# Kernel optimization log

Hardware: AMD Instinct MI355X
Metric: run time of the kernel (lower is better)

The kernel has to match this reference:

```python
import jax, jax.numpy as jnp
import numpy as np

B, T, C, H = 4, 2048, 1024, 16
D = C // H  # head_dim = 64


def setup_inputs() -> dict:
    key = jax.random.key(0)
    ks = jax.random.split(key, 5)
    s = 0.02
    return {
        "x": jax.random.normal(ks[0], (B, T, C), dtype=jnp.float32),
        "w_qkv": jax.random.normal(ks[1], (C, 3 * C), dtype=jnp.float32) * s,
        "b_qkv": jnp.zeros((3 * C,), dtype=jnp.float32),
        "w_proj": jax.random.normal(ks[2], (C, C), dtype=jnp.float32) * s,
        "b_proj": jnp.zeros((C,), dtype=jnp.float32),
    }


def reference(x, w_qkv, b_qkv, w_proj, b_proj):
    Bx, Tx, Cx = x.shape
    qkv = x @ w_qkv + b_qkv                      # [B,T,3C]
    q, k, v = jnp.split(qkv, 3, axis=-1)
    # [B,T,C] -> [B,H,T,D]
    q = q.reshape(Bx, Tx, H, D).transpose(0, 2, 1, 3)
    k = k.reshape(Bx, Tx, H, D).transpose(0, 2, 1, 3)
    v = v.reshape(Bx, Tx, H, D).transpose(0, 2, 1, 3)
    scale = 1.0 / np.sqrt(D).astype(np.float32)
    attn = jnp.einsum('bhqd,bhkd->bhqk', q, k) * scale   # [B,H,T,T]
    causal = jnp.tril(jnp.ones((Tx, Tx), dtype=bool))
    attn = jnp.where(causal[None, None], attn, -jnp.inf)
    attn = jax.nn.softmax(attn, axis=-1)
    out = jnp.einsum('bhqk,bhkd->bhqd', attn, v)          # [B,H,T,D]
    out = out.transpose(0, 2, 1, 3).reshape(Bx, Tx, Cx)   # [B,T,C]
    return out @ w_proj + b_proj
```

## Files before the change

kernel.cpp:

```cpp
#include <hip/hip_runtime.h>
#include <hip/hip_bf16.h>
#include <math.h>

using bf16 = __hip_bfloat16;
typedef __bf16 bf16x8 __attribute__((ext_vector_type(8)));
typedef float  f32x4  __attribute__((ext_vector_type(4)));
typedef unsigned short ushort8 __attribute__((ext_vector_type(8)));
typedef unsigned uint2v __attribute__((ext_vector_type(2)));

#define DEV __device__ __forceinline__

DEV void gld_lds16(const void* g, void* l) {
    __builtin_amdgcn_global_load_lds((const __attribute__((address_space(1))) void*)g,
                                     (__attribute__((address_space(3))) void*)l,
                                     16, 0, 0);
}

__global__ __launch_bounds__(256) void cast_f32_bf16(const float* __restrict__ in,
                                                     bf16* __restrict__ out, int n4) {
    int i = blockIdx.x * blockDim.x + threadIdx.x;
    if (i >= n4) return;
    float4 f = ((const float4*)in)[i];
    __align__(8) bf16 o[4] = {__float2bfloat16(f.x), __float2bfloat16(f.y),
                              __float2bfloat16(f.z), __float2bfloat16(f.w)};
    ((uint64_t*)out)[i] = *(const uint64_t*)o;
}

__global__ __launch_bounds__(256) void transpose_cast(const float* __restrict__ in,
                                                      bf16* __restrict__ out, int R, int Cn) {
    __shared__ float tile[32][33];
    int bx = blockIdx.x * 32;
    int by = blockIdx.y * 32;
    int tx = threadIdx.x & 31, ty = threadIdx.x >> 5;
    for (int i = ty; i < 32; i += 8)
        tile[i][tx] = in[(size_t)(by + i) * Cn + bx + tx];
    __syncthreads();
    for (int i = ty; i < 32; i += 8)
        out[(size_t)(bx + i) * R + by + tx] = __float2bfloat16(tile[tx][i]);
}

__global__ __launch_bounds__(256) void gemm_qkv(const bf16* __restrict__ A,
                                                const bf16* __restrict__ Bt,
                                                const float* __restrict__ bias,
                                                bf16* __restrict__ qb,
                                                bf16* __restrict__ kb,
                                                bf16* __restrict__ vTb) {
    constexpr int K = 1024, T = 2048;
    constexpr float CS = 0.18033688f;
    __shared__ __align__(16) bf16 Al[128 * 32];
    __shared__ __align__(16) bf16 Bl[128 * 32];
    __shared__ __align__(16) bf16 Et[32 * 136];
    int tid = threadIdx.x;
    int lane = tid & 63, w = tid >> 6;
    int wm = w >> 1, wn = w & 1;
    int l15 = lane & 15, quad = lane >> 4;
    int m0 = blockIdx.x * 128, n0 = blockIdx.y * 128;
    int l3 = l15 & 3;

    f32x4 acc[4][4] = {};
    for (int k0 = 0; k0 < K; k0 += 32) {
        __syncthreads();
        for (int it = 0; it < 2; ++it) {
            int e = (it * 256 + tid) * 8;
            int r = e >> 5, cu = (e >> 3) & 3;
            int cs = ((cu ^ (r & 3)) << 3);
            gld_lds16(A  + (size_t)(m0 + r) * K + k0 + cs, &Al[e]);
            gld_lds16(Bt + (size_t)(n0 + r) * K + k0 + cs, &Bl[e]);
        }
        __syncthreads();
        bf16x8 af[4], bfr[4];
        for (int i = 0; i < 4; ++i)
            af[i] = *(const bf16x8*)&Al[(wm * 64 + i * 16 + l15) * 32 + ((quad ^ l3) << 3)];
        for (int j = 0; j < 4; ++j)
            bfr[j] = *(const bf16x8*)&Bl[(wn * 64 + j * 16 + l15) * 32 + ((quad ^ l3) << 3)];
        for (int i = 0; i < 4; ++i)
            for (int j = 0; j < 4; ++j)
                acc[i][j] = __builtin_amdgcn_mfma_f32_16x16x32_bf16(af[i], bfr[j], acc[i][j], 0, 0, 0);
    }

    int mode = (blockIdx.y < 8) ? 0 : (blockIdx.y < 16 ? 1 : 2);
    float bv[4];
    for (int j = 0; j < 4; ++j)
        bv[j] = bias[n0 + wn * 64 + j * 16 + l15];
    float scl = (mode == 0) ? CS : 1.0f;

    for (int i = 0; i < 4; ++i) {
        __syncthreads();
        for (int j = 0; j < 4; ++j)
            for (int v = 0; v < 4; ++v)
                Et[(wm * 16 + quad * 4 + v) * 136 + wn * 64 + j * 16 + l15] =
                    __float2bfloat16((acc[i][j][v] + bv[j]) * scl);
        __syncthreads();
        if (mode < 2) {
            int r = tid >> 3, cc = (tid & 7) * 16;
            int m = m0 + i * 16 + (r < 16 ? r : r + 48);
            int b = m >> 11, t = m & 2047;
            int n = (n0 & 1023) + cc;
            int h = n >> 6, d = n & 63;
            bf16* dst = (mode == 0 ? qb : kb) + (((size_t)(b * 16 + h)) * T + t) * 64 + d;
            ushort8 u0 = *(const ushort8*)&Et[r * 136 + cc];
            ushort8 u1 = *(const ushort8*)&Et[r * 136 + cc + 8];
            *(ushort8*)dst = u0;
            *(ushort8*)(dst + 8) = u1;
        } else {
            int run = tid >> 7, d = tid & 127;
            int t0 = m0 + i * 16 + run * 64;
            int b = t0 >> 11, tt = t0 & 2047;
            int n = (n0 & 1023) + d;
            int h = n >> 6, dd = n & 63;
            __align__(16) bf16 tmp[16];
            for (int jj = 0; jj < 16; ++jj)
                tmp[jj] = Et[(run * 16 + jj) * 136 + d];
            bf16* dst = vTb + (((size_t)(b * 16 + h)) * 64 + dd) * T + tt;
            *(ushort8*)dst = *(const ushort8*)tmp;
            *(ushort8*)(dst + 8) = *(const ushort8*)(tmp + 8);
        }
    }
}

__global__ __launch_bounds__(256, 4) void flash_attn(const bf16* __restrict__ qb,
                                                     const bf16* __restrict__ kbuf,
                                                     const bf16* __restrict__ vT,
                                                     bf16* __restrict__ ob) {
    constexpr int T = 2048;
    __shared__ __align__(16) bf16 Kl[2][64 * 64];
    __shared__ __align__(16) bf16 Vl[64 * 64];
    __shared__ __align__(16) bf16 Pl[128 * 64];
    int tid = threadIdx.x;
    int lane = tid & 63, w = tid >> 6;
    int l15 = lane & 15, quad = lane >> 4;

    int g = blockIdx.x;
    int quarter = g >> 8;
    int j = (g >> 6) & 3;
    int bh = g & 63;
    int xq;
    switch (quarter) {
        case 0:  xq = 15 - j; break;
        case 1:  xq = 8 + j;  break;
        case 2:  xq = 4 + j;  break;
        default: xq = 3 - j;  break;
    }
    int q0 = xq << 7;
    const bf16* qbase = qb   + (size_t)bh * T * 64;
    const bf16* kbase = kbuf + (size_t)bh * T * 64;
    const bf16* vbase = vT   + (size_t)bh * 64 * T;

    int qg[2];
    bf16x8 qa[2][2];
#pragma unroll
    for (int s = 0; s < 2; ++s) {
        qg[s] = q0 + w * 32 + s * 16 + l15;
#pragma unroll
        for (int c = 0; c < 2; ++c)
            qa[s][c] = *(const bf16x8*)(qbase + (size_t)qg[s] * 64 + c * 32 + quad * 8);
    }

    bf16x8 ones;
#pragma unroll
    for (int i = 0; i < 8; ++i) ones[i] = (__bf16)1.0f;

    f32x4 O[2][4] = {};
    f32x4 O1[2] = {};
    int h7 = l15 & 7;

    int off0 = tid * 8, off1 = (256 + tid) * 8;
    int r0 = off0 >> 6, cb0 = (off0 >> 3) & 7;
    int r1 = off1 >> 6, cb1 = (off1 >> 3) & 7;
    int kc0 = (cb0 ^ (r0 & 7)) << 3, kc1 = (cb1 ^ (r1 & 7)) << 3;

    int prow0 = w * 32 + l15;
    int nit = 2 * xq + 2;

    bf16x8 vr0 = *(const bf16x8*)(vbase + (size_t)r0 * T + kc0);
    bf16x8 vr1 = *(const bf16x8*)(vbase + (size_t)r1 * T + kc1);
    gld_lds16(kbase + (size_t)r0 * 64 + kc0, &Kl[0][off0]);
    gld_lds16(kbase + (size_t)r1 * 64 + kc1, &Kl[0][off1]);
    *(bf16x8*)&Vl[off0] = vr0;
    *(bf16x8*)&Vl[off1] = vr1;

    for (int t = 0; t < nit; ++t) {
        int cur = t & 1;
        __syncthreads();
        bool pre = (t + 1 < nit);
        if (pre) {
            int kb2 = (t + 1) << 6, nxt = cur ^ 1;
            vr0 = *(const bf16x8*)(vbase + (size_t)r0 * T + kb2 + kc0);
            vr1 = *(const bf16x8*)(vbase + (size_t)r1 * T + kb2 + kc1);
            gld_lds16(kbase + (size_t)(kb2 + r0) * 64 + kc0, &Kl[nxt][off0]);
            gld_lds16(kbase + (size_t)(kb2 + r1) * 64 + kc1, &Kl[nxt][off1]);
        }
        int kb = t << 6;
        bool maskt = (t >= nit - 2);

#pragma unroll
        for (int jn = 0; jn < 4; ++jn) {
            int row = jn * 16 + l15;
            bf16x8 a0 = *(const bf16x8*)&Kl[cur][row * 64 + ((quad ^ h7) << 3)];
            bf16x8 a1 = *(const bf16x8*)&Kl[cur][row * 64 + (((4 + quad) ^ h7) << 3)];
            f32x4 sa[2] = {};
            __builtin_amdgcn_s_setprio(1);
            sa[0] = __builtin_amdgcn_mfma_f32_16x16x32_bf16(a0, qa[0][0], sa[0], 0, 0, 0);
            sa[0] = __builtin_amdgcn_mfma_f32_16x16x32_bf16(a1, qa[0][1], sa[0], 0, 0, 0);
            sa[1] = __builtin_amdgcn_mfma_f32_16x16x32_bf16(a0, qa[1][0], sa[1], 0, 0, 0);
            sa[1] = __builtin_amdgcn_mfma_f32_16x16x32_bf16(a1, qa[1][1], sa[1], 0, 0, 0);
            __builtin_amdgcn_s_setprio(0);
            int ubase = jn * 2 + (quad >> 1);
            int lowo = (quad & 1) << 2;
#pragma unroll
            for (int s = 0; s < 2; ++s) {
                float p[4];
#pragma unroll
                for (int v = 0; v < 4; ++v) {
                    float e = __builtin_amdgcn_exp2f(sa[s][v]);
                    if (maskt) {
                        int key = kb + jn * 16 + quad * 4 + v;
                        e = (key <= qg[s]) ? e : 0.f;
                    }
                    p[v] = e;
                }
                unsigned lo, hi;
                asm("v_cvt_pk_bf16_f32 %0, %1, %2" : "=v"(lo) : "v"(p[0]), "v"(p[1]));
                asm("v_cvt_pk_bf16_f32 %0, %1, %2" : "=v"(hi) : "v"(p[2]), "v"(p[3]));
                uint2v pv;
                pv[0] = lo;
                pv[1] = hi;
                int prow = prow0 + s * 16;
                *(uint2v*)&Pl[prow * 64 + ((ubase ^ h7) << 3) + lowo] = pv;
            }
        }
        asm volatile("s_waitcnt lgkmcnt(0)" ::: "memory");
        bf16x8 pf[2][2];
#pragma unroll
        for (int s = 0; s < 2; ++s) {
            int prow = prow0 + s * 16;
#pragma unroll
            for (int c = 0; c < 2; ++c)
                pf[s][c] = *(const bf16x8*)&Pl[prow * 64 + (((c * 4 + quad) ^ h7) << 3)];
        }

        __builtin_amdgcn_s_setprio(1);
#pragma unroll
        for (int s = 0; s < 2; ++s) {
            O1[s] = __builtin_amdgcn_mfma_f32_16x16x32_bf16(pf[s][0], ones, O1[s], 0, 0, 0);
            O1[s] = __builtin_amdgcn_mfma_f32_16x16x32_bf16(pf[s][1], ones, O1[s], 0, 0, 0);
        }
        __builtin_amdgcn_s_setprio(0);

#pragma unroll
        for (int jd = 0; jd < 4; ++jd) {
            int vrow = jd * 16 + l15;
            bf16x8 v0 = *(const bf16x8*)&Vl[vrow * 64 + ((quad ^ h7) << 3)];
            bf16x8 v1 = *(const bf16x8*)&Vl[vrow * 64 + (((4 + quad) ^ h7) << 3)];
            __builtin_amdgcn_s_setprio(1);
            O[0][jd] = __builtin_amdgcn_mfma_f32_16x16x32_bf16(pf[0][0], v0, O[0][jd], 0, 0, 0);
            O[0][jd] = __builtin_amdgcn_mfma_f32_16x16x32_bf16(pf[0][1], v1, O[0][jd], 0, 0, 0);
            O[1][jd] = __builtin_amdgcn_mfma_f32_16x16x32_bf16(pf[1][0], v0, O[1][jd], 0, 0, 0);
            O[1][jd] = __builtin_amdgcn_mfma_f32_16x16x32_bf16(pf[1][1], v1, O[1][jd], 0, 0, 0);
            __builtin_amdgcn_s_setprio(0);
        }

        __builtin_amdgcn_s_barrier();
        if (pre) {
            *(bf16x8*)&Vl[off0] = vr0;
            *(bf16x8*)&Vl[off1] = vr1;
        }
    }

    int b = bh >> 4, h = bh & 15;
#pragma unroll
    for (int s = 0; s < 2; ++s) {
        float linv[4];
#pragma unroll
        for (int v = 0; v < 4; ++v) linv[v] = 1.f / O1[s][v];
#pragma unroll
        for (int jd = 0; jd < 4; ++jd) {
#pragma unroll
            for (int v = 0; v < 4; ++v) {
                int qr = q0 + w * 32 + s * 16 + quad * 4 + v;
                ob[((size_t)(b * T + qr)) * 1024 + h * 64 + jd * 16 + l15] =
                    __float2bfloat16(O[s][jd][v] * linv[v]);
            }
        }
    }
}

__global__ __launch_bounds__(256) void gemm_proj(const bf16* __restrict__ A,
                                                 const bf16* __restrict__ Bt,
                                                 const float* __restrict__ bias,
                                                 float* __restrict__ out) {
    constexpr int K = 1024, N = 1024;
    __shared__ __align__(16) bf16 Al[128 * 32];
    __shared__ __align__(16) bf16 Bl[128 * 32];
    int tid = threadIdx.x;
    int lane = tid & 63, w = tid >> 6;
    int wm = w >> 1, wn = w & 1;
    int l15 = lane & 15, quad = lane >> 4;
    int m0 = blockIdx.x * 128, n0 = blockIdx.y * 128;
    int l3 = l15 & 3;

    f32x4 acc[4][4] = {};
    for (int k0 = 0; k0 < K; k0 += 32) {
        __syncthreads();
        for (int it = 0; it < 2; ++it) {
            int e = (it * 256 + tid) * 8;
            int r = e >> 5, cu = (e >> 3) & 3;
            int cs = ((cu ^ (r & 3)) << 3);
            gld_lds16(A  + (size_t)(m0 + r) * K + k0 + cs, &Al[e]);
            gld_lds16(Bt + (size_t)(n0 + r) * K + k0 + cs, &Bl[e]);
        }
        __syncthreads();
        bf16x8 af[4], bfr[4];
        for (int i = 0; i < 4; ++i)
            af[i] = *(const bf16x8*)&Al[(wm * 64 + i * 16 + l15) * 32 + ((quad ^ l3) << 3)];
        for (int j = 0; j < 4; ++j)
            bfr[j] = *(const bf16x8*)&Bl[(wn * 64 + j * 16 + l15) * 32 + ((quad ^ l3) << 3)];
        for (int i = 0; i < 4; ++i)
            for (int j = 0; j < 4; ++j)
                acc[i][j] = __builtin_amdgcn_mfma_f32_16x16x32_bf16(af[i], bfr[j], acc[i][j], 0, 0, 0);
    }
    for (int i = 0; i < 4; ++i) {
        int mbase = m0 + wm * 64 + i * 16 + quad * 4;
        for (int j = 0; j < 4; ++j) {
            int n = n0 + wn * 64 + j * 16 + l15;
            float bv = bias[n];
            for (int v = 0; v < 4; ++v)
                out[(size_t)(mbase + v) * N + n] = acc[i][j][v] + bv;
        }
    }
}

extern "C" void kernel_launch(void* const* d_in, const int* in_sizes, int n_in,
                              void* d_out, int out_size, void* d_ws, size_t ws_size,
                              hipStream_t stream) {
    (void)in_sizes; (void)n_in; (void)out_size; (void)ws_size;
    const float* x      = (const float*)d_in[0];
    const float* w_qkv  = (const float*)d_in[1];
    const float* b_qkv  = (const float*)d_in[2];
    const float* w_proj = (const float*)d_in[3];
    const float* b_proj = (const float*)d_in[4];
    float* out = (float*)d_out;

    char* ws = (char*)d_ws;
    bf16* xb     = (bf16*)(ws);
    bf16* wqkvT  = (bf16*)(ws + (16u << 20));
    bf16* wprojT = (bf16*)(ws + (22u << 20));
    bf16* qbuf   = (bf16*)(ws + (24u << 20));
    bf16* kbuf   = (bf16*)(ws + (40u << 20));
    bf16* vTb    = (bf16*)(ws + (72u << 20));
    bf16* ob     = (bf16*)(ws + (56u << 20));

    cast_f32_bf16<<<8192, 256, 0, stream>>>(x, xb, 8192 * 1024 / 4);
    transpose_cast<<<dim3(3072 / 32, 1024 / 32), 256, 0, stream>>>(w_qkv, wqkvT, 1024, 3072);
    transpose_cast<<<dim3(1024 / 32, 1024 / 32), 256, 0, stream>>>(w_proj, wprojT, 1024, 1024);
    gemm_qkv<<<dim3(64, 24), 256, 0, stream>>>(xb, wqkvT, b_qkv, qbuf, kbuf, vTb);
    flash_attn<<<1024, 256, 0, stream>>>(qbuf, kbuf, vTb, ob);
    gemm_proj<<<dim3(64, 8), 256, 0, stream>>>(ob, wprojT, b_proj, out);
}
```

Measured before the change: 245.2 us.

## Double-buffer LDS tiles in QKV and projection GEMM main loops

Both GEMM kernels now keep two LDS buffers per operand and prefetch the next K-slice with async global-to-LDS loads while MFMAs run on the current slice. This drops one barrier per iteration and is meant to hide global load latency behind compute. In exchange it doubles the LDS tile footprint, which may lower occupancy. The compiler may also insert conservative vmcnt waits before the LDS reads, which would limit the overlap.

```diff
diff --git a/kernel.cpp b/kernel.cpp
--- a/kernel.cpp
+++ b/kernel.cpp
@@ -47,8 +47,8 @@
                                                 bf16* __restrict__ vTb) {
     constexpr int K = 1024, T = 2048;
     constexpr float CS = 0.18033688f;
-    __shared__ __align__(16) bf16 Al[128 * 32];
-    __shared__ __align__(16) bf16 Bl[128 * 32];
+    __shared__ __align__(16) bf16 Al[2][128 * 32];
+    __shared__ __align__(16) bf16 Bl[2][128 * 32];
     __shared__ __align__(16) bf16 Et[32 * 136];
     int tid = threadIdx.x;
     int lane = tid & 63, w = tid >> 6;
@@ -57,22 +57,31 @@
     int m0 = blockIdx.x * 128, n0 = blockIdx.y * 128;
     int l3 = l15 & 3;
 
+    int e0 = tid * 8, e1 = (256 + tid) * 8;
+    int r0 = e0 >> 5, cs0 = ((((e0 >> 3) & 3) ^ (r0 & 3)) << 3);
+    int r1 = e1 >> 5, cs1 = ((((e1 >> 3) & 3) ^ (r1 & 3)) << 3);
+
     f32x4 acc[4][4] = {};
-    for (int k0 = 0; k0 < K; k0 += 32) {
-        __syncthreads();
-        for (int it = 0; it < 2; ++it) {
-            int e = (it * 256 + tid) * 8;
-            int r = e >> 5, cu = (e >> 3) & 3;
-            int cs = ((cu ^ (r & 3)) << 3);
-            gld_lds16(A  + (size_t)(m0 + r) * K + k0 + cs, &Al[e]);
-            gld_lds16(Bt + (size_t)(n0 + r) * K + k0 + cs, &Bl[e]);
-        }
-        __syncthreads();
+    gld_lds16(A  + (size_t)(m0 + r0) * K + cs0, &Al[0][e0]);
+    gld_lds16(Bt + (size_t)(n0 + r0) * K + cs0, &Bl[0][e0]);
+    gld_lds16(A  + (size_t)(m0 + r1) * K + cs1, &Al[0][e1]);
+    gld_lds16(Bt + (size_t)(n0 + r1) * K + cs1, &Bl[0][e1]);
+
+    for (int t = 0; t < K / 32; ++t) {
+        int cur = t & 1;
+        __syncthreads();
+        if (t + 1 < K / 32) {
+            int k2 = (t + 1) * 32, nxt = cur ^ 1;
+            gld_lds16(A  + (size_t)(m0 + r0) * K + k2 + cs0, &Al[nxt][e0]);
+            gld_lds16(Bt + (size_t)(n0 + r0) * K + k2 + cs0, &Bl[nxt][e0]);
+            gld_lds16(A  + (size_t)(m0 + r1) * K + k2 + cs1, &Al[nxt][e1]);
+            gld_lds16(Bt + (size_t)(n0 + r1) * K + k2 + cs1, &Bl[nxt][e1]);
+        }
         bf16x8 af[4], bfr[4];
         for (int i = 0; i < 4; ++i)
-            af[i] = *(const bf16x8*)&Al[(wm * 64 + i * 16 + l15) * 32 + ((quad ^ l3) << 3)];
+            af[i] = *(const bf16x8*)&Al[cur][(wm * 64 + i * 16 + l15) * 32 + ((quad ^ l3) << 3)];
         for (int j = 0; j < 4; ++j)
-            bfr[j] = *(const bf16x8*)&Bl[(wn * 64 + j * 16 + l15) * 32 + ((quad ^ l3) << 3)];
+            bfr[j] = *(const bf16x8*)&Bl[cur][(wn * 64 + j * 16 + l15) * 32 + ((quad ^ l3) << 3)];
         for (int i = 0; i < 4; ++i)
             for (int j = 0; j < 4; ++j)
                 acc[i][j] = __builtin_amdgcn_mfma_f32_16x16x32_bf16(af[i], bfr[j], acc[i][j], 0, 0, 0);
@@ -290,8 +299,8 @@
                                                  const float* __restrict__ bias,
                                                  float* __restrict__ out) {
     constexpr int K = 1024, N = 1024;
-    __shared__ __align__(16) bf16 Al[128 * 32];
-    __shared__ __align__(16) bf16 Bl[128 * 32];
+    __shared__ __align__(16) bf16 Al[2][128 * 32];
+    __shared__ __align__(16) bf16 Bl[2][128 * 32];
     int tid = threadIdx.x;
     int lane = tid & 63, w = tid >> 6;
     int wm = w >> 1, wn = w & 1;
@@ -299,22 +308,31 @@
     int m0 = blockIdx.x * 128, n0 = blockIdx.y * 128;
     int l3 = l15 & 3;
 
+    int e0 = tid * 8, e1 = (256 + tid) * 8;
+    int r0 = e0 >> 5, cs0 = ((((e0 >> 3) & 3) ^ (r0 & 3)) << 3);
+    int r1 = e1 >> 5, cs1 = ((((e1 >> 3) & 3) ^ (r1 & 3)) << 3);
+
     f32x4 acc[4][4] = {};
-    for (int k0 = 0; k0 < K; k0 += 32) {
-        __syncthreads();
-        for (int it = 0; it < 2; ++it) {
-            int e = (it * 256 + tid) * 8;
-            int r = e >> 5, cu = (e >> 3) & 3;
-            int cs = ((cu ^ (r & 3)) << 3);
-            gld_lds16(A  + (size_t)(m0 + r) * K + k0 + cs, &Al[e]);
-            gld_lds16(Bt + (size_t)(n0 + r) * K + k0 + cs, &Bl[e]);
-        }
-        __syncthreads();
+    gld_lds16(A  + (size_t)(m0 + r0) * K + cs0, &Al[0][e0]);
+    gld_lds16(Bt + (size_t)(n0 + r0) * K + cs0, &Bl[0][e0]);
+    gld_lds16(A  + (size_t)(m0 + r1) * K + cs1, &Al[0][e1]);
+    gld_lds16(Bt + (size_t)(n0 + r1) * K + cs1, &Bl[0][e1]);
+
+    for (int t = 0; t < K / 32; ++t) {
+        int cur = t & 1;
+        __syncthreads();
+        if (t + 1 < K / 32) {
+            int k2 = (t + 1) * 32, nxt = cur ^ 1;
+            gld_lds16(A  + (size_t)(m0 + r0) * K + k2 + cs0, &Al[nxt][e0]);
+            gld_lds16(Bt + (size_t)(n0 + r0) * K + k2 + cs0, &Bl[nxt][e0]);
+            gld_lds16(A  + (size_t)(m0 + r1) * K + k2 + cs1, &Al[nxt][e1]);
+            gld_lds16(Bt + (size_t)(n0 + r1) * K + k2 + cs1, &Bl[nxt][e1]);
+        }
         bf16x8 af[4], bfr[4];
         for (int i = 0; i < 4; ++i)
-            af[i] = *(const bf16x8*)&Al[(wm * 64 + i * 16 + l15) * 32 + ((quad ^ l3) << 3)];
+            af[i] = *(const bf16x8*)&Al[cur][(wm * 64 + i * 16 + l15) * 32 + ((quad ^ l3) << 3)];
         for (int j = 0; j < 4; ++j)
-            bfr[j] = *(const bf16x8*)&Bl[(wn * 64 + j * 16 + l15) * 32 + ((quad ^ l3) << 3)];
+            bfr[j] = *(const bf16x8*)&Bl[cur][(wn * 64 + j * 16 + l15) * 32 + ((quad ^ l3) << 3)];
         for (int i = 0; i < 4; ++i)
             for (int j = 0; j < 4; ++j)
                 acc[i][j] = __builtin_amdgcn_mfma_f32_16x16x32_bf16(af[i], bfr[j], acc[i][j], 0, 0, 0);
```

After: 260.0 us. +6.0%, slower.
